# Kernel tuning notes

Measured on AMD Instinct MI355X. Metric: run time of the kernel, lower is better.

The kernel has to match this reference:

```python
import math
import jax, jax.numpy as jnp
import numpy as np

EMBED_DIM = 1024
NUM_HEADS = 16
HEAD_DIM = EMBED_DIM // NUM_HEADS
BLOCK_LEN = 128  # local_radius + 1
NUM_BUCKETS = 32
MAX_DISTANCE = 128


def _relative_position_bucket(relative_position, num_buckets=NUM_BUCKETS, max_distance=MAX_DISTANCE):
    # bidirectional=True (encoder / is_decoder=False)
    num_buckets //= 2
    relative_buckets = (relative_position > 0).astype(jnp.int32) * num_buckets
    relative_position = jnp.abs(relative_position)
    max_exact = num_buckets // 2
    is_small = relative_position < max_exact
    rp_safe = jnp.maximum(relative_position, 1).astype(jnp.float32)
    rp_if_large = max_exact + (
        jnp.log(rp_safe / max_exact) / math.log(max_distance / max_exact) * (num_buckets - max_exact)
    ).astype(jnp.int32)
    rp_if_large = jnp.minimum(rp_if_large, num_buckets - 1)
    relative_buckets = relative_buckets + jnp.where(is_small, relative_position, rp_if_large)
    return relative_buckets


def _compute_bias(rel_bias_table, block_len):
    # memory positions over 3 concatenated blocks; context = middle block
    memory_position = jnp.arange(3 * block_len, dtype=jnp.int32)
    context_position = memory_position[block_len:-block_len]
    relative_position = memory_position[None, :] - context_position[:, None]  # [L, 3L]
    buckets = _relative_position_bucket(relative_position)
    values = rel_bias_table[buckets]                      # [L, 3L, H]
    values = jnp.transpose(values, (2, 0, 1))[None, None]  # [1, 1, H, L, 3L]
    return values


def _concat_3_blocks(x):
    # x: [B, nb, L, H, D] -> [B, nb, 3L, H, D]
    xp = jnp.pad(x, ((0, 0), (1, 1), (0, 0), (0, 0), (0, 0)))
    nb = x.shape[1]
    return jnp.concatenate([xp[:, i:i + nb] for i in range(3)], axis=2)


def setup_inputs() -> dict:
    key = jax.random.key(0)
    k0, k1, k2, k3, k4, k5 = jax.random.split(key, 6)
    T, B = 4096, 4
    scale_in = 1.0 / math.sqrt(EMBED_DIM)
    return {
        "hidden_states": jax.random.normal(k0, (T, B, EMBED_DIM), dtype=jnp.float32),
        "Wq": jax.random.normal(k1, (EMBED_DIM, EMBED_DIM), dtype=jnp.float32) * scale_in,
        "Wk": jax.random.normal(k2, (EMBED_DIM, EMBED_DIM), dtype=jnp.float32) * scale_in,
        "Wv": jax.random.normal(k3, (EMBED_DIM, EMBED_DIM), dtype=jnp.float32) * scale_in,
        "Wo": jax.random.normal(k4, (EMBED_DIM, EMBED_DIM), dtype=jnp.float32) * scale_in,
        "rel_bias_table": jax.random.normal(k5, (NUM_BUCKETS, NUM_HEADS), dtype=jnp.float32) * 0.1,
    }


def reference(hidden_states, Wq, Wk, Wv, Wo, rel_bias_table):
    # hidden_states: [T, B, C] -> [B, T, C]
    x = jnp.transpose(hidden_states, (1, 0, 2))
    B, T, C = x.shape
    L = BLOCK_LEN
    scaling = HEAD_DIM ** (-0.5)

    def shape_heads(y):
        return y.reshape(B, T, NUM_HEADS, HEAD_DIM)

    q = shape_heads(x @ Wq) * scaling
    k = shape_heads(x @ Wk)
    v = shape_heads(x @ Wv)

    # split into blocks (T assumed multiple of L here; original pads otherwise)
    nb = T // L
    q = q.reshape(B, nb, L, NUM_HEADS, HEAD_DIM)
    k = k.reshape(B, nb, L, NUM_HEADS, HEAD_DIM)
    v = v.reshape(B, nb, L, NUM_HEADS, HEAD_DIM)

    k3 = _concat_3_blocks(k)  # [B, nb, 3L, H, D]
    v3 = _concat_3_blocks(v)

    scores = jnp.einsum('bnqhd,bnkhd->bnhqk', q, k3)  # [B, nb, H, L, 3L]
    position_bias = _compute_bias(rel_bias_table, L)
    scores = scores + position_bias

    attn = jax.nn.softmax(scores.astype(jnp.float32), axis=-1).astype(scores.dtype)
    out = jnp.einsum('bnhqk,bnkhd->bnqhd', attn, v3)  # [B, nb, L, H, D]
    out = out.reshape(B, T, EMBED_DIM)[:, :T]
    out = out @ Wo
    return jnp.transpose(out, (1, 0, 2))  # [T, B, C]
```

## Files before the change

kernel.cpp:

```cpp
#include <hip/hip_runtime.h>
#include <hip/hip_bf16.h>


#define T_LEN 4096
#define BATCH 4
#define CDIM 1024
#define NHEAD 16
#define HDIM 64
#define BLK 128
#define NBLK 32

typedef __attribute__((ext_vector_type(8))) short bf16x8;
typedef __attribute__((ext_vector_type(4))) float f32x4;

__device__ __forceinline__ unsigned short f2b(float f) {
    __hip_bfloat16 h = __float2bfloat16(f);
    return *reinterpret_cast<unsigned short*>(&h);
}
__device__ __forceinline__ void gl_lds16(const void* g, void* l) {
    __builtin_amdgcn_global_load_lds(
        (const __attribute__((address_space(1))) unsigned int*)g,
        (__attribute__((address_space(3))) unsigned int*)l, 16, 0, 0);
}

__global__ __launch_bounds__(256) void conv_x(const float* __restrict__ hidden,
                                              unsigned short* __restrict__ xb) {
    int chunk = blockIdx.x * 256 + threadIdx.x;
    int c8 = chunk & 127;
    int rem = chunk >> 7;
    int b = rem & 3;
    int t = rem >> 2;
    const float* src = hidden + ((size_t)rem << 10) + c8 * 8;
    float4 v0 = *(const float4*)src;
    float4 v1 = *(const float4*)(src + 4);
    bf16x8 o;
    o[0] = (short)f2b(v0.x); o[1] = (short)f2b(v0.y);
    o[2] = (short)f2b(v0.z); o[3] = (short)f2b(v0.w);
    o[4] = (short)f2b(v1.x); o[5] = (short)f2b(v1.y);
    o[6] = (short)f2b(v1.z); o[7] = (short)f2b(v1.w);
    *(bf16x8*)&xb[((size_t)(b * T_LEN + t) << 10) + c8 * 8] = o;
}

__global__ __launch_bounds__(256) void conv_w(
    const float* __restrict__ W0, const float* __restrict__ W1,
    const float* __restrict__ W2, const float* __restrict__ W3,
    unsigned short* __restrict__ wt)
{
    const int z = blockIdx.z;
    const float* W = (z == 0) ? W0 : (z == 1) ? W1 : (z == 2) ? W2 : W3;
    const float scale = (z == 0) ? 0.125f : 1.0f;
    unsigned short* hi = wt + (size_t)z * (CDIM * CDIM);
    __shared__ float tile[32][33];
    const int r = threadIdx.x >> 5;
    const int c = threadIdx.x & 31;
    const int k0 = blockIdx.x * 32;
    const int n0 = blockIdx.y * 32;
#pragma unroll
    for (int i = 0; i < 4; ++i)
        tile[r + i * 8][c] = W[(size_t)(k0 + r + i * 8) * CDIM + n0 + c] * scale;
    __syncthreads();
#pragma unroll
    for (int i = 0; i < 4; ++i) {
        int nn = r + i * 8;
        hi[(size_t)(n0 + nn) * CDIM + k0 + c] = f2b(tile[c][nn]);
    }
}


#define STAGE(pb, tau, half, isB) do {                                         \
    const unsigned short* _gb = (isB) ? Bg : Ag;                               \
    const int _bo = (pb) * 32768 + (isB) * 16384 + (half) * 8192;              \
    gl_lds16(_gb + (size_t)((half) * 128 + sr) * 1024 + (tau) * 64,            \
             (short*)lds + _bo + ldsW);                                        \
    gl_lds16(_gb + (size_t)((half) * 128 + 64 + sr) * 1024 + (tau) * 64,       \
             (short*)lds + _bo + 4096 + ldsW);                                 \
} while (0)

#define LDB(p) do {                                                            \
    _Pragma("unroll") for (int nr = 0; nr < 4; ++nr) {                         \
        int _row = wc * 64 + nr * 16 + li;                                     \
        _Pragma("unroll") for (int ks = 0; ks < 2; ++ks)                       \
            bkf[nr][ks] = *(const bf16x8*)(ldsc + (p) * 65536 + 32768 +        \
                ((_row * 128 + ks * 64 + g * 16) ^ swz));                      \
    } } while (0)

#define LDA(p, q) do {                                                         \
    _Pragma("unroll") for (int dm = 0; dm < 2; ++dm) {                         \
        int _row = wr * 128 + ((q) * 2 + dm) * 16 + li;                        \
        _Pragma("unroll") for (int ks = 0; ks < 2; ++ks)                       \
            af[dm][ks] = *(const bf16x8*)(ldsc + (p) * 65536 +                 \
                ((_row * 128 + ks * 64 + g * 16) ^ swz));                      \
    } } while (0)

#define MM(q) do {                                                             \
    _Pragma("unroll") for (int dm = 0; dm < 2; ++dm)                           \
    _Pragma("unroll") for (int nr = 0; nr < 4; ++nr) {                         \
        acc[(q)*2+dm][nr] = __builtin_amdgcn_mfma_f32_16x16x32_bf16(           \
            af[dm][0], bkf[nr][0], acc[(q)*2+dm][nr], 0, 0, 0);                \
        acc[(q)*2+dm][nr] = __builtin_amdgcn_mfma_f32_16x16x32_bf16(           \
            af[dm][1], bkf[nr][1], acc[(q)*2+dm][nr], 0, 0, 0);                \
    } } while (0)

#define MID() do {                                                             \
    __builtin_amdgcn_s_barrier();                                              \
    asm volatile("s_waitcnt lgkmcnt(0)" ::: "memory");                         \
    __builtin_amdgcn_sched_barrier(0);                                         \
    __builtin_amdgcn_s_setprio(1);                                             \
} while (0)

#define TAIL() do {                                                            \
    __builtin_amdgcn_s_setprio(0);                                             \
    __builtin_amdgcn_sched_barrier(0);                                         \
    __builtin_amdgcn_s_barrier();                                              \
} while (0)

template<int MODE>
__global__ __launch_bounds__(512, 1) void gemm_8ph(
    const unsigned short* __restrict__ Am,
    const unsigned short* __restrict__ Bm,
    unsigned short* __restrict__ qb, unsigned short* __restrict__ kb,
    unsigned short* __restrict__ vb, float* __restrict__ fout)
{
    __shared__ short lds[65536];

    const int tid = threadIdx.x;
    const int w = tid >> 6, lane = tid & 63;
    const int g = lane >> 4, li = lane & 15;
    const int wr = w >> 2, wc = w & 3;
    const int m0 = blockIdx.x * 256;
    const int n0 = blockIdx.y * 256;

    const int sr = tid >> 3;
    const int cbs = ((tid & 7) * 16) ^ ((sr & 7) << 4);
    const int ldsW = w * 512;
    const unsigned short* Ag = Am + (size_t)m0 * 1024 + (cbs >> 1);
    const unsigned short* Bg = Bm + (size_t)n0 * 1024 + (cbs >> 1);

    const char* ldsc = (const char*)lds;
    const int swz = (li & 7) << 4;

    f32x4 acc[8][4];
#pragma unroll
    for (int a = 0; a < 8; ++a)
#pragma unroll
        for (int b = 0; b < 4; ++b) acc[a][b] = (f32x4){0.f, 0.f, 0.f, 0.f};

    bf16x8 bkf[4][2];
    bf16x8 af[2][2];

    STAGE(0, 0, 0, 0); STAGE(0, 0, 1, 0);
    STAGE(0, 0, 0, 1); STAGE(0, 0, 1, 1);
    STAGE(1, 1, 0, 1); STAGE(1, 1, 1, 1);
    asm volatile("s_waitcnt vmcnt(4)" ::: "memory");
    __builtin_amdgcn_s_barrier();

#pragma unroll 1
    for (int i = 0; i < 8; ++i) {
        const int o = 2 * i + 1, e2 = 2 * i + 2, o2 = 2 * i + 3;
        const bool pf = (i < 7);
        LDB(0); LDA(0, 0); STAGE(1, o, 0, 0); MID(); MM(0); TAIL();
        LDA(0, 1); STAGE(1, o, 1, 0); MID(); MM(1); TAIL();
        LDA(0, 2); if (pf) STAGE(0, e2, 0, 1); MID(); MM(2); TAIL();
        LDA(0, 3); if (pf) STAGE(0, e2, 1, 1); MID(); MM(3);
        __builtin_amdgcn_s_setprio(0);
        __builtin_amdgcn_sched_barrier(0);
        if (pf) asm volatile("s_waitcnt vmcnt(4)" ::: "memory");
        else    asm volatile("s_waitcnt vmcnt(0)" ::: "memory");
        __builtin_amdgcn_s_barrier();
        LDB(1); LDA(1, 0); if (pf) STAGE(0, e2, 0, 0); MID(); MM(0); TAIL();
        LDA(1, 1); if (pf) STAGE(0, e2, 1, 0); MID(); MM(1); TAIL();
        LDA(1, 2); if (pf) STAGE(1, o2, 0, 1); MID(); MM(2); TAIL();
        LDA(1, 3); if (pf) STAGE(1, o2, 1, 1); MID(); MM(3);
        __builtin_amdgcn_s_setprio(0);
        __builtin_amdgcn_sched_barrier(0);
        if (pf) asm volatile("s_waitcnt vmcnt(4)" ::: "memory");
        else    asm volatile("s_waitcnt vmcnt(0)" ::: "memory");
        __builtin_amdgcn_s_barrier();
    }

    if (MODE == 0) {
        const int nA = n0 + wc * 64;
        const int z = nA >> 10;
        const int hh = (nA & 1023) >> 6;
        unsigned short* ob = (z == 0) ? qb : (z == 1) ? kb : vb;
#pragma unroll
        for (int mr = 0; mr < 8; ++mr)
#pragma unroll
            for (int reg = 0; reg < 4; ++reg) {
                int m = m0 + wr * 128 + mr * 16 + g * 4 + reg;
                size_t ro = ((size_t)((m >> 12) * NHEAD + hh) * T_LEN + (m & 4095)) * HDIM;
#pragma unroll
                for (int nr = 0; nr < 4; ++nr)
                    ob[ro + nr * 16 + li] = f2b(acc[mr][nr][reg]);
            }
    } else {
#pragma unroll
        for (int mr = 0; mr < 8; ++mr)
#pragma unroll
            for (int reg = 0; reg < 4; ++reg) {
                int m = m0 + wr * 128 + mr * 16 + g * 4 + reg;
                float* orow = fout + ((size_t)(m & 4095) * BATCH + (m >> 12)) * CDIM
                              + n0 + wc * 64;
#pragma unroll
                for (int nr = 0; nr < 4; ++nr)
                    orow[nr * 16 + li] = acc[mr][nr][reg];
            }
    }
}

__device__ __forceinline__ int rel_bucket(int rel) {
    int rb = (rel > 0) ? 16 : 0;
    int rp = abs(rel);
    int bu;
    if (rp < 8) bu = rp;
    else if (rp < 12) bu = 8;
    else if (rp < 16) bu = 9;
    else if (rp < 23) bu = 10;
    else if (rp < 32) bu = 11;
    else if (rp < 46) bu = 12;
    else if (rp < 64) bu = 13;
    else if (rp < 91) bu = 14;
    else bu = 15;
    return rb + bu;
}

#define QS_STR 72
#define KS_STR 72
#define VT_STR 72
#define PL_STR 72

__global__ __launch_bounds__(256) void attn_mfma(
    const unsigned short* __restrict__ qb, const unsigned short* __restrict__ kb,
    const unsigned short* __restrict__ vb, const float* __restrict__ table,
    unsigned short* __restrict__ ao)
{
    const int n = blockIdx.x;
    const int h = blockIdx.y;
    const int b = blockIdx.z;
    const int tid = threadIdx.x;
    const int w = tid >> 6;
    const int lane = tid & 63;
    const int g = lane >> 4;
    const int li = lane & 15;

    __shared__ short Qs[128 * QS_STR];
    __shared__ short Ks[64 * KS_STR];
    __shared__ short Vt[64 * VT_STR];
    __shared__ short Pl[4][32 * PL_STR];
    __shared__ float ldsb[512];

    const unsigned short* qBase = qb + (((size_t)b * NHEAD + h) * T_LEN + (size_t)n * BLK) * HDIM;
    const unsigned short* kBase = kb + ((size_t)b * NHEAD + h) * T_LEN * HDIM;
    const unsigned short* vBase = vb + ((size_t)b * NHEAD + h) * T_LEN * HDIM;

    for (int i = tid; i < 512; i += 256) {
        ldsb[i] = table[rel_bucket(i - 255) * NHEAD + h];
    }
#pragma unroll
    for (int u = 0; u < 4; ++u) {
        int c = tid + u * 256;
        int row = c >> 3, ch = c & 7;
        *(bf16x8*)&Qs[row * QS_STR + ch * 8] =
            *(const bf16x8*)(qBase + (size_t)row * HDIM + ch * 8);
    }
    __syncthreads();

    bf16x8 aq[2][2];
#pragma unroll
    for (int mi = 0; mi < 2; ++mi)
#pragma unroll
        for (int ks = 0; ks < 2; ++ks)
            aq[mi][ks] = *(bf16x8*)&Qs[(w * 32 + mi * 16 + li) * QS_STR + ks * 32 + g * 8];

    f32x4 oacc[2][4];
    float m_run[2][4], l_run[2][4], scl[2][4];
#pragma unroll
    for (int mi = 0; mi < 2; ++mi)
#pragma unroll
        for (int r4 = 0; r4 < 4; ++r4) {
            oacc[mi][r4] = (f32x4){0.f, 0.f, 0.f, 0.f};
            m_run[mi][r4] = -1e30f;
            l_run[mi][r4] = 0.f;
        }

    for (int kt = 0; kt < 6; ++kt) {
        __syncthreads();
        const int tk0 = (n - 1) * BLK + kt * 64;
#pragma unroll
        for (int u = 0; u < 2; ++u) {
            int c = tid + u * 256;
            int row = c >> 3, ch = c & 7;
            int tok = tk0 + row;
            bf16x8 kv = {0, 0, 0, 0, 0, 0, 0, 0};
            bf16x8 vv = {0, 0, 0, 0, 0, 0, 0, 0};
            if (tok >= 0 && tok < T_LEN) {
                kv = *(const bf16x8*)(kBase + (size_t)tok * HDIM + ch * 8);
                vv = *(const bf16x8*)(vBase + (size_t)tok * HDIM + ch * 8);
            }
            *(bf16x8*)&Ks[row * KS_STR + ch * 8] = kv;
#pragma unroll
            for (int j = 0; j < 8; ++j)
                Vt[(ch * 8 + j) * VT_STR + row] = vv[j];
        }
        __syncthreads();

        f32x4 sacc[2][4];
#pragma unroll
        for (int mi = 0; mi < 2; ++mi)
#pragma unroll
            for (int ni = 0; ni < 4; ++ni)
                sacc[mi][ni] = (f32x4){0.f, 0.f, 0.f, 0.f};
#pragma unroll
        for (int ks = 0; ks < 2; ++ks) {
            bf16x8 bk[4];
#pragma unroll
            for (int ni = 0; ni < 4; ++ni)
                bk[ni] = *(bf16x8*)&Ks[(ni * 16 + li) * KS_STR + ks * 32 + g * 8];
#pragma unroll
            for (int mi = 0; mi < 2; ++mi)
#pragma unroll
                for (int ni = 0; ni < 4; ++ni)
                    sacc[mi][ni] = __builtin_amdgcn_mfma_f32_16x16x32_bf16(
                        aq[mi][ks], bk[ni], sacc[mi][ni], 0, 0, 0);
        }

#pragma unroll
        for (int mi = 0; mi < 2; ++mi) {
            const int rq = w * 32 + mi * 16 + g * 4;
#pragma unroll
            for (int reg = 0; reg < 4; ++reg) {
                const int r = rq + reg;
                float sv[4];
#pragma unroll
                for (int ni = 0; ni < 4; ++ni) {
                    int kk = kt * 64 + ni * 16 + li;
                    sv[ni] = sacc[mi][ni][reg] + ldsb[kk - r + 127];
                }
                float tm = fmaxf(fmaxf(sv[0], sv[1]), fmaxf(sv[2], sv[3]));
                tm = fmaxf(tm, __shfl_xor(tm, 1));
                tm = fmaxf(tm, __shfl_xor(tm, 2));
                tm = fmaxf(tm, __shfl_xor(tm, 4));
                tm = fmaxf(tm, __shfl_xor(tm, 8));
                float mold = m_run[mi][reg];
                float mnew = fmaxf(mold, tm);
                float sc = __expf(mold - mnew);
                float ps = 0.f;
                unsigned short pb[4];
#pragma unroll
                for (int ni = 0; ni < 4; ++ni) {
                    float pv = __expf(sv[ni] - mnew);
                    ps += pv;
                    pb[ni] = f2b(pv);
                }
                ps += __shfl_xor(ps, 1);
                ps += __shfl_xor(ps, 2);
                ps += __shfl_xor(ps, 4);
                ps += __shfl_xor(ps, 8);
                l_run[mi][reg] = l_run[mi][reg] * sc + ps;
                m_run[mi][reg] = mnew;
                scl[mi][reg] = sc;
#pragma unroll
                for (int ni = 0; ni < 4; ++ni)
                    Pl[w][(mi * 16 + g * 4 + reg) * PL_STR + ni * 16 + li] = (short)pb[ni];
            }
        }
#pragma unroll
        for (int mi = 0; mi < 2; ++mi)
#pragma unroll
            for (int dn = 0; dn < 4; ++dn)
#pragma unroll
                for (int reg = 0; reg < 4; ++reg)
                    oacc[mi][dn][reg] *= scl[mi][reg];

        __syncthreads();

#pragma unroll
        for (int ks = 0; ks < 2; ++ks) {
            bf16x8 ap[2], bv[4];
#pragma unroll
            for (int mi = 0; mi < 2; ++mi)
                ap[mi] = *(bf16x8*)&Pl[w][(mi * 16 + li) * PL_STR + ks * 32 + g * 8];
#pragma unroll
            for (int dn = 0; dn < 4; ++dn)
                bv[dn] = *(bf16x8*)&Vt[(dn * 16 + li) * VT_STR + ks * 32 + g * 8];
#pragma unroll
            for (int mi = 0; mi < 2; ++mi)
#pragma unroll
                for (int dn = 0; dn < 4; ++dn)
                    oacc[mi][dn] = __builtin_amdgcn_mfma_f32_16x16x32_bf16(
                        ap[mi], bv[dn], oacc[mi][dn], 0, 0, 0);
        }
    }

#pragma unroll
    for (int mi = 0; mi < 2; ++mi) {
#pragma unroll
        for (int reg = 0; reg < 4; ++reg) {
            float inv = 1.f / l_run[mi][reg];
            int t = n * BLK + w * 32 + mi * 16 + g * 4 + reg;
            unsigned short* orow = ao + ((size_t)b * T_LEN + t) * CDIM + h * HDIM;
#pragma unroll
            for (int dn = 0; dn < 4; ++dn)
                orow[dn * 16 + li] = f2b(oacc[mi][dn][reg] * inv);
        }
    }
}

extern "C" void kernel_launch(void* const* d_in, const int* in_sizes, int n_in,
                              void* d_out, int out_size, void* d_ws, size_t ws_size,
                              hipStream_t stream) {
    const float* hidden = (const float*)d_in[0];
    const float* Wq = (const float*)d_in[1];
    const float* Wk = (const float*)d_in[2];
    const float* Wv = (const float*)d_in[3];
    const float* Wo = (const float*)d_in[4];
    const float* table = (const float*)d_in[5];
    float* out = (float*)d_out;

    const size_t qkvElems = (size_t)BATCH * NHEAD * T_LEN * HDIM;
    const size_t wElems = (size_t)CDIM * CDIM;
    const size_t needed = (4 * qkvElems + 4 * wElems) * 2;
    if (ws_size < needed) return;

    unsigned short* qb = (unsigned short*)d_ws;
    unsigned short* kb = qb + qkvElems;
    unsigned short* vb = kb + qkvElems;
    unsigned short* xb = vb + qkvElems;
    unsigned short* wt = xb + qkvElems;

    conv_w<<<dim3(32, 32, 4), 256, 0, stream>>>(Wq, Wk, Wv, Wo, wt);
    conv_x<<<8192, 256, 0, stream>>>(hidden, xb);
    gemm_8ph<0><<<dim3(64, 12), 512, 0, stream>>>(xb, wt, qb, kb, vb, nullptr);
    attn_mfma<<<dim3(NBLK, NHEAD, BATCH), 256, 0, stream>>>(qb, kb, vb, table, xb);
    gemm_8ph<1><<<dim3(64, 4), 512, 0, stream>>>(xb, wt + 3 * wElems,
                                                 nullptr, nullptr, nullptr, out);
}
```

Before: 272.6 us.

## Produce transposed V from a separate GEMM and read K/V directly from global in attention

The V projection is split into its own GEMM launch that computes W_v·x^T and writes V already transposed per head (dim-major over tokens). The attention kernel then loads Q, K and V^T fragments straight from global memory into registers instead of staging them through LDS. This removes the LDS staging, the scalar transpose into Vt and several block-wide barriers per key tile. It also skips out-of-range key tiles and raises wave priority around the MFMAs. The trade-offs are an extra kernel launch, strided transposed stores in the V GEMM, and uncoalesced global fragment loads that are repeated across the four waves.

```diff
diff --git a/kernel.cpp b/kernel.cpp
--- a/kernel.cpp
+++ b/kernel.cpp
@@ -119,7 +119,7 @@
     const unsigned short* __restrict__ Am,
     const unsigned short* __restrict__ Bm,
     unsigned short* __restrict__ qb, unsigned short* __restrict__ kb,
-    unsigned short* __restrict__ vb, float* __restrict__ fout)
+    unsigned short* __restrict__ vT, float* __restrict__ fout)
 {
     __shared__ short lds[65536];
 
@@ -180,9 +180,8 @@
 
     if (MODE == 0) {
         const int nA = n0 + wc * 64;
-        const int z = nA >> 10;
         const int hh = (nA & 1023) >> 6;
-        unsigned short* ob = (z == 0) ? qb : (z == 1) ? kb : vb;
+        unsigned short* ob = ((nA >> 10) == 0) ? qb : kb;
 #pragma unroll
         for (int mr = 0; mr < 8; ++mr)
 #pragma unroll
@@ -193,7 +192,7 @@
                 for (int nr = 0; nr < 4; ++nr)
                     ob[ro + nr * 16 + li] = f2b(acc[mr][nr][reg]);
             }
-    } else {
+    } else if (MODE == 1) {
 #pragma unroll
         for (int mr = 0; mr < 8; ++mr)
 #pragma unroll
@@ -204,6 +203,19 @@
 #pragma unroll
                 for (int nr = 0; nr < 4; ++nr)
                     orow[nr * 16 + li] = acc[mr][nr][reg];
+            }
+    } else {
+#pragma unroll
+        for (int mr = 0; mr < 8; ++mr)
+#pragma unroll
+            for (int reg = 0; reg < 4; ++reg) {
+                int m = m0 + wr * 128 + mr * 16 + g * 4 + reg;
+#pragma unroll
+                for (int nr = 0; nr < 4; ++nr) {
+                    int nn = n0 + wc * 64 + nr * 16 + li;
+                    vT[((size_t)((nn >> 12) * 1024 + m) << 12) + (nn & 4095)] =
+                        f2b(acc[mr][nr][reg]);
+                }
             }
     }
 }
@@ -224,14 +236,11 @@
     return rb + bu;
 }
 
-#define QS_STR 72
-#define KS_STR 72
-#define VT_STR 72
 #define PL_STR 72
 
 __global__ __launch_bounds__(256) void attn_mfma(
     const unsigned short* __restrict__ qb, const unsigned short* __restrict__ kb,
-    const unsigned short* __restrict__ vb, const float* __restrict__ table,
+    const unsigned short* __restrict__ vT, const float* __restrict__ table,
     unsigned short* __restrict__ ao)
 {
     const int n = blockIdx.x;
@@ -243,34 +252,25 @@
     const int g = lane >> 4;
     const int li = lane & 15;
 
-    __shared__ short Qs[128 * QS_STR];
-    __shared__ short Ks[64 * KS_STR];
-    __shared__ short Vt[64 * VT_STR];
     __shared__ short Pl[4][32 * PL_STR];
     __shared__ float ldsb[512];
 
-    const unsigned short* qBase = qb + (((size_t)b * NHEAD + h) * T_LEN + (size_t)n * BLK) * HDIM;
+    for (int i = tid; i < 512; i += 256)
+        ldsb[i] = table[rel_bucket(i - 255) * NHEAD + h];
+    __syncthreads();
+
+    const unsigned short* qBase =
+        qb + (((size_t)b * NHEAD + h) * T_LEN + (size_t)n * BLK) * HDIM;
     const unsigned short* kBase = kb + ((size_t)b * NHEAD + h) * T_LEN * HDIM;
-    const unsigned short* vBase = vb + ((size_t)b * NHEAD + h) * T_LEN * HDIM;
-
-    for (int i = tid; i < 512; i += 256) {
-        ldsb[i] = table[rel_bucket(i - 255) * NHEAD + h];
-    }
-#pragma unroll
-    for (int u = 0; u < 4; ++u) {
-        int c = tid + u * 256;
-        int row = c >> 3, ch = c & 7;
-        *(bf16x8*)&Qs[row * QS_STR + ch * 8] =
-            *(const bf16x8*)(qBase + (size_t)row * HDIM + ch * 8);
-    }
-    __syncthreads();
+    const unsigned short* vTBase = vT + ((size_t)b * NHEAD + h) * (size_t)HDIM * T_LEN;
 
     bf16x8 aq[2][2];
 #pragma unroll
     for (int mi = 0; mi < 2; ++mi)
 #pragma unroll
         for (int ks = 0; ks < 2; ++ks)
-            aq[mi][ks] = *(bf16x8*)&Qs[(w * 32 + mi * 16 + li) * QS_STR + ks * 32 + g * 8];
+            aq[mi][ks] = *(const bf16x8*)(qBase +
+                (size_t)(w * 32 + mi * 16 + li) * HDIM + ks * 32 + g * 8);
 
     f32x4 oacc[2][4];
     float m_run[2][4], l_run[2][4], scl[2][4];
@@ -284,25 +284,8 @@
         }
 
     for (int kt = 0; kt < 6; ++kt) {
-        __syncthreads();
         const int tk0 = (n - 1) * BLK + kt * 64;
-#pragma unroll
-        for (int u = 0; u < 2; ++u) {
-            int c = tid + u * 256;
-            int row = c >> 3, ch = c & 7;
-            int tok = tk0 + row;
-            bf16x8 kv = {0, 0, 0, 0, 0, 0, 0, 0};
-            bf16x8 vv = {0, 0, 0, 0, 0, 0, 0, 0};
-            if (tok >= 0 && tok < T_LEN) {
-                kv = *(const bf16x8*)(kBase + (size_t)tok * HDIM + ch * 8);
-                vv = *(const bf16x8*)(vBase + (size_t)tok * HDIM + ch * 8);
-            }
-            *(bf16x8*)&Ks[row * KS_STR + ch * 8] = kv;
-#pragma unroll
-            for (int j = 0; j < 8; ++j)
-                Vt[(ch * 8 + j) * VT_STR + row] = vv[j];
-        }
-        __syncthreads();
+        const bool inb = (tk0 >= 0) && (tk0 < T_LEN);
 
         f32x4 sacc[2][4];
 #pragma unroll
@@ -310,18 +293,23 @@
 #pragma unroll
             for (int ni = 0; ni < 4; ++ni)
                 sacc[mi][ni] = (f32x4){0.f, 0.f, 0.f, 0.f};
-#pragma unroll
-        for (int ks = 0; ks < 2; ++ks) {
-            bf16x8 bk[4];
-#pragma unroll
-            for (int ni = 0; ni < 4; ++ni)
-                bk[ni] = *(bf16x8*)&Ks[(ni * 16 + li) * KS_STR + ks * 32 + g * 8];
-#pragma unroll
-            for (int mi = 0; mi < 2; ++mi)
+        if (inb) {
+            __builtin_amdgcn_s_setprio(1);
+#pragma unroll
+            for (int ks = 0; ks < 2; ++ks) {
+                bf16x8 bk[4];
 #pragma unroll
                 for (int ni = 0; ni < 4; ++ni)
-                    sacc[mi][ni] = __builtin_amdgcn_mfma_f32_16x16x32_bf16(
-                        aq[mi][ks], bk[ni], sacc[mi][ni], 0, 0, 0);
+                    bk[ni] = *(const bf16x8*)(kBase +
+                        (size_t)(tk0 + ni * 16 + li) * HDIM + ks * 32 + g * 8);
+#pragma unroll
+                for (int mi = 0; mi < 2; ++mi)
+#pragma unroll
+                    for (int ni = 0; ni < 4; ++ni)
+                        sacc[mi][ni] = __builtin_amdgcn_mfma_f32_16x16x32_bf16(
+                            aq[mi][ks], bk[ni], sacc[mi][ni], 0, 0, 0);
+            }
+            __builtin_amdgcn_s_setprio(0);
         }
 
 #pragma unroll
@@ -372,23 +360,26 @@
                 for (int reg = 0; reg < 4; ++reg)
                     oacc[mi][dn][reg] *= scl[mi][reg];
 
-        __syncthreads();
-
-#pragma unroll
-        for (int ks = 0; ks < 2; ++ks) {
-            bf16x8 ap[2], bv[4];
-#pragma unroll
-            for (int mi = 0; mi < 2; ++mi)
-                ap[mi] = *(bf16x8*)&Pl[w][(mi * 16 + li) * PL_STR + ks * 32 + g * 8];
-#pragma unroll
-            for (int dn = 0; dn < 4; ++dn)
-                bv[dn] = *(bf16x8*)&Vt[(dn * 16 + li) * VT_STR + ks * 32 + g * 8];
-#pragma unroll
-            for (int mi = 0; mi < 2; ++mi)
+        if (inb) {
+            __builtin_amdgcn_s_setprio(1);
+#pragma unroll
+            for (int ks = 0; ks < 2; ++ks) {
+                bf16x8 ap[2], bv[4];
+#pragma unroll
+                for (int mi = 0; mi < 2; ++mi)
+                    ap[mi] = *(bf16x8*)&Pl[w][(mi * 16 + li) * PL_STR + ks * 32 + g * 8];
 #pragma unroll
                 for (int dn = 0; dn < 4; ++dn)
-                    oacc[mi][dn] = __builtin_amdgcn_mfma_f32_16x16x32_bf16(
-                        ap[mi], bv[dn], oacc[mi][dn], 0, 0, 0);
+                    bv[dn] = *(const bf16x8*)(vTBase +
+                        (size_t)(dn * 16 + li) * T_LEN + tk0 + ks * 32 + g * 8);
+#pragma unroll
+                for (int mi = 0; mi < 2; ++mi)
+#pragma unroll
+                    for (int dn = 0; dn < 4; ++dn)
+                        oacc[mi][dn] = __builtin_amdgcn_mfma_f32_16x16x32_bf16(
+                            ap[mi], bv[dn], oacc[mi][dn], 0, 0, 0);
+            }
+            __builtin_amdgcn_s_setprio(0);
         }
     }
 
@@ -424,14 +415,16 @@
 
     unsigned short* qb = (unsigned short*)d_ws;
     unsigned short* kb = qb + qkvElems;
-    unsigned short* vb = kb + qkvElems;
-    unsigned short* xb = vb + qkvElems;
+    unsigned short* vT = kb + qkvElems;
+    unsigned short* xb = vT + qkvElems;
     unsigned short* wt = xb + qkvElems;
 
     conv_w<<<dim3(32, 32, 4), 256, 0, stream>>>(Wq, Wk, Wv, Wo, wt);
     conv_x<<<8192, 256, 0, stream>>>(hidden, xb);
-    gemm_8ph<0><<<dim3(64, 12), 512, 0, stream>>>(xb, wt, qb, kb, vb, nullptr);
-    attn_mfma<<<dim3(NBLK, NHEAD, BATCH), 256, 0, stream>>>(qb, kb, vb, table, xb);
+    gemm_8ph<0><<<dim3(64, 8), 512, 0, stream>>>(xb, wt, qb, kb, nullptr, nullptr);
+    gemm_8ph<2><<<dim3(4, 64), 512, 0, stream>>>(wt + 2 * wElems, xb,
+                                                 nullptr, nullptr, vT, nullptr);
+    attn_mfma<<<dim3(NBLK, NHEAD, BATCH), 256, 0, stream>>>(qb, kb, vT, table, xb);
     gemm_8ph<1><<<dim3(64, 4), 512, 0, stream>>>(xb, wt + 3 * wElems,
                                                  nullptr, nullptr, nullptr, out);
 }
```

Result: slower. 293.4 us (+7.7%).
